# Kernel tuning notes

Hardware: AMD Instinct MI355X
Metric: run time of the kernel (lower is better)

## Reference

```python
import jax, jax.numpy as jnp
import numpy as np

EMBED_DIM = 1024
HEADS = 16
D_HEAD = EMBED_DIM // HEADS
B, S = 4, 2048


def setup_inputs() -> dict:
    key = jax.random.key(0)
    ks = jax.random.split(key, 7)
    scale = 1.0 / np.sqrt(EMBED_DIM)
    inp = {
        "key": jax.random.normal(ks[0], (B, S, EMBED_DIM), jnp.float32),
        "query": jax.random.normal(ks[1], (B, S, EMBED_DIM), jnp.float32),
        "value": jax.random.normal(ks[2], (B, S, EMBED_DIM), jnp.float32),
        # causal boolean mask, broadcastable to [B, H, S, S]
        "mask": jnp.tril(jnp.ones((S, S), dtype=bool))[None, None, :, :] * jnp.ones((B, 1, 1, 1), dtype=bool),
        # nn.Linear weights, stored torch-style as [out_features, in_features]
        "Wq": jax.random.normal(ks[3], (EMBED_DIM, EMBED_DIM), jnp.float32) * scale,
        "Wk": jax.random.normal(ks[4], (EMBED_DIM, EMBED_DIM), jnp.float32) * scale,
        "Wv": jax.random.normal(ks[5], (EMBED_DIM, EMBED_DIM), jnp.float32) * scale,
        "Wo": jax.random.normal(ks[6], (EMBED_DIM, EMBED_DIM), jnp.float32) * scale,
    }
    return inp


def reference(key, query, value, mask, Wq, Wk, Wv, Wo):
    # projections (nn.Linear, bias=False): x @ W.T
    q = query @ Wq.T                                    # [B,S,E]
    k = key @ Wk.T
    v = value @ Wv.T
    # split heads -> [B,H,S,d]
    def split(x):
        return x.reshape(B, S, HEADS, D_HEAD).transpose(0, 2, 1, 3)
    q, k, v = split(q), split(k), split(v)
    # scaled dot-product scores [B,H,S,S]
    scores = jnp.einsum("bhqd,bhkd->bhqk", q, k) / np.sqrt(D_HEAD).astype(np.float32)
    scores = jnp.where(mask, scores, jnp.float32(-1e9))
    attn = jax.nn.softmax(scores, axis=-1)
    # attention output, merge heads
    out = jnp.einsum("bhqk,bhkd->bhqd", attn, v)        # [B,H,S,d]
    out = out.transpose(0, 2, 1, 3).reshape(B, S, EMBED_DIM)
    return out @ Wo.T
```

## Files before the change

kernel.cpp:

```cpp
#include <hip/hip_runtime.h>

#define SEQ 2048
#define EMBED 1024
#define DHEAD 64

typedef _Float16 h8 __attribute__((ext_vector_type(8)));
typedef _Float16 h4 __attribute__((ext_vector_type(4)));
typedef float f4 __attribute__((ext_vector_type(4)));
typedef unsigned int u32;

__device__ __forceinline__ void gload_lds16(const void* g, void* l) {
    __builtin_amdgcn_global_load_lds(
        (const __attribute__((address_space(1))) u32*)g,
        (__attribute__((address_space(3))) u32*)l, 16, 0, 0);
}

__global__ __launch_bounds__(256) void cvt_f16(
    const float* __restrict__ q, const float* __restrict__ k, const float* __restrict__ v,
    const float* __restrict__ wq, const float* __restrict__ wk, const float* __restrict__ wv,
    const float* __restrict__ wo,
    _Float16* __restrict__ q16, _Float16* __restrict__ k16, _Float16* __restrict__ v16,
    _Float16* __restrict__ wq16, _Float16* __restrict__ wk16, _Float16* __restrict__ wv16,
    _Float16* __restrict__ wo16)
{
    int bid = blockIdx.x;
    const float* src;
    _Float16* dst;
    float scale = 1.0f;
    size_t base;
    if (bid < 24576) {
        int seg = bid >> 13;
        base = (size_t)(bid & 8191) * 1024 + threadIdx.x * 4;
        src = seg == 0 ? q : seg == 1 ? k : v;
        dst = seg == 0 ? q16 : seg == 1 ? k16 : v16;
    } else {
        int wb = bid - 24576;
        int seg = wb >> 10;
        base = (size_t)(wb & 1023) * 1024 + threadIdx.x * 4;
        src = seg == 0 ? wq : seg == 1 ? wk : seg == 2 ? wv : wo;
        dst = seg == 0 ? wq16 : seg == 1 ? wk16 : seg == 2 ? wv16 : wo16;
        if (seg == 0) scale = 0.18033688011112042f;
    }
    float4 x = *(const float4*)(src + base);
    h4 y = { (_Float16)(x.x * scale), (_Float16)(x.y * scale),
             (_Float16)(x.z * scale), (_Float16)(x.w * scale) };
    *(h4*)(dst + base) = y;
}

__device__ __forceinline__ void gemm_core(const _Float16* __restrict__ A, const _Float16* __restrict__ W,
                                          int m0, int n0, int tid,
                                          _Float16* As, _Float16* Bs, f4 acc[4][4])
{
    const int lane = tid & 63, wave = tid >> 6;
    const int t16 = lane & 15, quad = lane >> 4;
    const int wm = (wave >> 1) * 64, wn = (wave & 1) * 64;
    const int wb = wave * 64;
    const int u0 = tid, u1 = tid + 256;
    const int r0 = u0 >> 2, c0 = u0 & 3;
    const int r1 = u1 >> 2, c1 = u1 & 3;
    const _Float16* ga0 = A + (size_t)(m0 + r0) * 1024 + c0 * 8;
    const _Float16* ga1 = A + (size_t)(m0 + r1) * 1024 + c1 * 8;
    const _Float16* gb0 = W + (size_t)(n0 + r0) * 1024 + c0 * 8;
    const _Float16* gb1 = W + (size_t)(n0 + r1) * 1024 + c1 * 8;
    _Float16* la0 = As + wb * 8;
    _Float16* la1 = As + (256 + wb) * 8;
    _Float16* lb0 = Bs + wb * 8;
    _Float16* lb1 = Bs + (256 + wb) * 8;

    for (int k0 = 0; k0 < 1024; k0 += 32) {
        __syncthreads();
        gload_lds16(ga0 + k0, la0);
        gload_lds16(ga1 + k0, la1);
        gload_lds16(gb0 + k0, lb0);
        gload_lds16(gb1 + k0, lb1);
        __syncthreads();
        h8 af[4], bf[4];
#pragma unroll
        for (int i = 0; i < 4; ++i)
            af[i] = *(const h8*)(As + (wm + i * 16 + t16) * 32 + quad * 8);
#pragma unroll
        for (int j = 0; j < 4; ++j)
            bf[j] = *(const h8*)(Bs + (wn + j * 16 + t16) * 32 + quad * 8);
#pragma unroll
        for (int i = 0; i < 4; ++i)
#pragma unroll
            for (int j = 0; j < 4; ++j)
                acc[i][j] = __builtin_amdgcn_mfma_f32_16x16x32_f16(af[i], bf[j], acc[i][j], 0, 0, 0);
    }
}

__global__ __launch_bounds__(256) void proj_qkv(
    const _Float16* __restrict__ q16, const _Float16* __restrict__ k16, const _Float16* __restrict__ v16,
    const _Float16* __restrict__ Wq, const _Float16* __restrict__ Wk, const _Float16* __restrict__ Wv,
    _Float16* __restrict__ Qh, _Float16* __restrict__ Kh, _Float16* __restrict__ Vt)
{
    __shared__ _Float16 As[4096], Bs[4096];
    const int tid = threadIdx.x;
    const int z = blockIdx.z;
    const _Float16 *A, *W;
    int m0, n0;
    if (z == 2) { A = Wv; W = v16; m0 = blockIdx.y * 128; n0 = blockIdx.x * 128; }
    else if (z == 0) { A = q16; W = Wq; m0 = blockIdx.x * 128; n0 = blockIdx.y * 128; }
    else { A = k16; W = Wk; m0 = blockIdx.x * 128; n0 = blockIdx.y * 128; }

    f4 acc[4][4];
    const f4 z4 = {0.f, 0.f, 0.f, 0.f};
#pragma unroll
    for (int i = 0; i < 4; ++i)
#pragma unroll
        for (int j = 0; j < 4; ++j) acc[i][j] = z4;

    gemm_core(A, W, m0, n0, tid, As, Bs, acc);

    const int lane = tid & 63, wave = tid >> 6;
    const int t16 = lane & 15, quad = lane >> 4;
    const int wm = (wave >> 1) * 64, wn = (wave & 1) * 64;
#pragma unroll
    for (int i = 0; i < 4; ++i)
#pragma unroll
        for (int j = 0; j < 4; ++j)
#pragma unroll
            for (int reg = 0; reg < 4; ++reg) {
                int gm = m0 + wm + i * 16 + quad * 4 + reg;
                int gn = n0 + wn + j * 16 + t16;
                float vv = acc[i][j][reg];
                if (z < 2) {
                    int b = gm >> 11, s = gm & 2047, h = gn >> 6, dd = gn & 63;
                    _Float16* dst = (z == 0) ? Qh : Kh;
                    dst[(((size_t)(b * 16 + h) * SEQ) + s) * DHEAD + dd] = (_Float16)vv;
                } else {
                    int h = gm >> 6, dd = gm & 63, b = gn >> 11, s = gn & 2047;
                    Vt[(((size_t)(b * 16 + h) * DHEAD) + dd) * SEQ + s] = (_Float16)vv;
                }
            }
}

__global__ __launch_bounds__(256) void attn3(
    const _Float16* __restrict__ Qh, const _Float16* __restrict__ Kh,
    const _Float16* __restrict__ Vt, _Float16* __restrict__ Ob)
{
    __shared__ _Float16 Kbuf[2][8][512];
    __shared__ _Float16 Vbuf[2][8][512];
    __shared__ _Float16 Pex[4][2][512];

    const int tid = threadIdx.x;
    const int lane = tid & 63, wave = tid >> 6;
    const int t16 = lane & 15, quad = lane >> 4;
    const int bh = blockIdx.x;
    const int b = bh >> 4, h = bh & 15;
    const int qb = (gridDim.y - 1) - blockIdx.y;
    const int q0 = qb * 128;
    const int nqt = qb * 2 + 2;

    const _Float16* Qp = Qh + (size_t)bh * SEQ * DHEAD;
    const _Float16* Kp = Kh + (size_t)bh * SEQ * DHEAD;
    const _Float16* Vp = Vt + (size_t)bh * DHEAD * SEQ;

    const int qlo[2] = { q0 + wave * 32, q0 + wave * 32 + 16 };
    const int last0 = (qlo[0] + 15) >> 6;

    h8 qf[2][2];
#pragma unroll
    for (int qb2 = 0; qb2 < 2; ++qb2)
#pragma unroll
        for (int kc = 0; kc < 2; ++kc)
            qf[qb2][kc] = *(const h8*)(Qp + (size_t)(qlo[qb2] + t16) * 64 + kc * 32 + quad * 8);

    const _Float16* Kl = Kp + t16 * 64 + quad * 8;
    const _Float16* Vl = Vp + t16 * 2048 + quad * 8;

#define STAGE(jt_, bufi)                                                                  \
    do {                                                                                  \
        if (wave < 2) {                                                                   \
            _Pragma("unroll")                                                             \
            for (int i_ = 0; i_ < 4; ++i_) {                                              \
                int g_ = wave * 4 + i_;                                                   \
                gload_lds16(Kl + (jt_) * 4096 + (g_ >> 1) * 1024 + (g_ & 1) * 32,         \
                            &Kbuf[bufi][g_][0]);                                          \
            }                                                                             \
        } else {                                                                          \
            _Pragma("unroll")                                                             \
            for (int i_ = 0; i_ < 4; ++i_) {                                              \
                int g_ = (wave - 2) * 4 + i_;                                             \
                gload_lds16(Vl + (g_ >> 1) * 32768 + (jt_) * 64 + (g_ & 1) * 32,          \
                            &Vbuf[bufi][g_][0]);                                          \
            }                                                                             \
        }                                                                                 \
    } while (0)

    STAGE(0, 0);
    __syncthreads();

    float mv[2] = {-1e30f, -1e30f};
    float lv[2] = {0.f, 0.f};
    f4 o_acc[2][4];
    const f4 z4 = {0.f, 0.f, 0.f, 0.f};
#pragma unroll
    for (int qb2 = 0; qb2 < 2; ++qb2)
#pragma unroll
        for (int dt = 0; dt < 4; ++dt) o_acc[qb2][dt] = z4;

    for (int jt = 0; jt < nqt; ++jt) {
        const int buf = jt & 1;
        if (jt + 1 < nqt) STAGE(jt + 1, buf ^ 1);

        if (jt <= last0) {
            f4 s0[4], s1[4];
#pragma unroll
            for (int j4 = 0; j4 < 4; ++j4) {
                h8 kfa = *(const h8*)(&Kbuf[buf][j4 * 2 + 0][lane * 8]);
                h8 kfb = *(const h8*)(&Kbuf[buf][j4 * 2 + 1][lane * 8]);
                s1[j4] = __builtin_amdgcn_mfma_f32_16x16x32_f16(kfa, qf[1][0], z4, 0, 0, 0);
                s1[j4] = __builtin_amdgcn_mfma_f32_16x16x32_f16(kfb, qf[1][1], s1[j4], 0, 0, 0);
                s0[j4] = __builtin_amdgcn_mfma_f32_16x16x32_f16(kfa, qf[0][0], z4, 0, 0, 0);
                s0[j4] = __builtin_amdgcn_mfma_f32_16x16x32_f16(kfb, qf[0][1], s0[j4], 0, 0, 0);
            }

            auto softmax_store = [&](f4* s, int qb2) {
                const int myq = qlo[qb2] + t16;
                if ((jt << 6) + 63 > qlo[qb2]) {
#pragma unroll
                    for (int j4 = 0; j4 < 4; ++j4)
#pragma unroll
                        for (int reg = 0; reg < 4; ++reg) {
                            int kk = (jt << 6) + j4 * 16 + quad * 4 + reg;
                            if (kk > myq) s[j4][reg] = -1e30f;
                        }
                }
                float mr = s[0][0];
#pragma unroll
                for (int j4 = 0; j4 < 4; ++j4)
#pragma unroll
                    for (int reg = 0; reg < 4; ++reg) mr = fmaxf(mr, s[j4][reg]);
                mr = fmaxf(mr, __shfl_xor(mr, 16, 64));
                mr = fmaxf(mr, __shfl_xor(mr, 32, 64));
                float mn = mv[qb2];
                if (__any(mr > mn + 8.0f)) {
                    mn = fmaxf(mn, mr);
                    float al = __builtin_amdgcn_exp2f(mv[qb2] - mn);
                    mv[qb2] = mn;
                    lv[qb2] *= al;
#pragma unroll
                    for (int dt = 0; dt < 4; ++dt)
#pragma unroll
                        for (int reg = 0; reg < 4; ++reg) o_acc[qb2][dt][reg] *= al;
                }
                float rs = 0.f;
#pragma unroll
                for (int j4 = 0; j4 < 4; ++j4) {
#pragma unroll
                    for (int reg = 0; reg < 4; ++reg) {
                        float p = __builtin_amdgcn_exp2f(s[j4][reg] - mn);
                        s[j4][reg] = p;
                        rs += p;
                    }
                    int Lt = (((j4 & 1) * 2 + (quad >> 1)) << 4) + t16;
                    h4 ph = { (_Float16)s[j4][0], (_Float16)s[j4][1],
                              (_Float16)s[j4][2], (_Float16)s[j4][3] };
                    *(h4*)(&Pex[wave][j4 >> 1][Lt * 8 + (quad & 1) * 4]) = ph;
                }
                rs += __shfl_xor(rs, 16, 64);
                rs += __shfl_xor(rs, 32, 64);
                lv[qb2] += rs;
            };

            softmax_store(s0, 0);
            {
                h8 pa = *(const h8*)(&Pex[wave][0][lane * 8]);
                h8 pb = *(const h8*)(&Pex[wave][1][lane * 8]);
#pragma unroll
                for (int dt = 0; dt < 4; ++dt) {
                    h8 ava = *(const h8*)(&Vbuf[buf][dt * 2 + 0][lane * 8]);
                    h8 avb = *(const h8*)(&Vbuf[buf][dt * 2 + 1][lane * 8]);
                    o_acc[0][dt] = __builtin_amdgcn_mfma_f32_16x16x32_f16(ava, pa, o_acc[0][dt], 0, 0, 0);
                    o_acc[0][dt] = __builtin_amdgcn_mfma_f32_16x16x32_f16(avb, pb, o_acc[0][dt], 0, 0, 0);
                }
            }
            softmax_store(s1, 1);
            {
                h8 pa = *(const h8*)(&Pex[wave][0][lane * 8]);
                h8 pb = *(const h8*)(&Pex[wave][1][lane * 8]);
#pragma unroll
                for (int dt = 0; dt < 4; ++dt) {
                    h8 ava = *(const h8*)(&Vbuf[buf][dt * 2 + 0][lane * 8]);
                    h8 avb = *(const h8*)(&Vbuf[buf][dt * 2 + 1][lane * 8]);
                    o_acc[1][dt] = __builtin_amdgcn_mfma_f32_16x16x32_f16(ava, pa, o_acc[1][dt], 0, 0, 0);
                    o_acc[1][dt] = __builtin_amdgcn_mfma_f32_16x16x32_f16(avb, pb, o_acc[1][dt], 0, 0, 0);
                }
            }
        }
        __syncthreads();
    }

#pragma unroll
    for (int qb2 = 0; qb2 < 2; ++qb2) {
        float inv = __builtin_amdgcn_rcpf(lv[qb2]);
        _Float16* ep = &Pex[wave][0][0];
#pragma unroll
        for (int dt = 0; dt < 4; ++dt) {
            h4 ov = { (_Float16)(o_acc[qb2][dt][0] * inv), (_Float16)(o_acc[qb2][dt][1] * inv),
                      (_Float16)(o_acc[qb2][dt][2] * inv), (_Float16)(o_acc[qb2][dt][3] * inv) };
            *(h4*)(ep + t16 * 64 + dt * 16 + quad * 4) = ov;
        }
        h8 r0 = *(const h8*)(ep + t16 * 64 + quad * 8);
        h8 r1 = *(const h8*)(ep + t16 * 64 + 32 + quad * 8);
        int s = qlo[qb2] + t16;
        _Float16* og = Ob + ((size_t)(b * SEQ + s)) * EMBED + h * DHEAD;
        *(h8*)(og + quad * 8) = r0;
        *(h8*)(og + 32 + quad * 8) = r1;
    }
#undef STAGE
}

__global__ __launch_bounds__(256) void proj_out(
    const _Float16* __restrict__ A, const _Float16* __restrict__ Wo, float* __restrict__ out)
{
    __shared__ _Float16 As[4096], Bs[4096];
    const int tid = threadIdx.x;
    const int m0 = blockIdx.x * 128, n0 = blockIdx.y * 128;
    f4 acc[4][4];
    const f4 z4 = {0.f, 0.f, 0.f, 0.f};
#pragma unroll
    for (int i = 0; i < 4; ++i)
#pragma unroll
        for (int j = 0; j < 4; ++j) acc[i][j] = z4;

    gemm_core(A, Wo, m0, n0, tid, As, Bs, acc);

    const int lane = tid & 63, wave = tid >> 6;
    const int t16 = lane & 15, quad = lane >> 4;
    const int wm = (wave >> 1) * 64, wn = (wave & 1) * 64;
#pragma unroll
    for (int i = 0; i < 4; ++i)
#pragma unroll
        for (int j = 0; j < 4; ++j)
#pragma unroll
            for (int reg = 0; reg < 4; ++reg) {
                int gm = m0 + wm + i * 16 + quad * 4 + reg;
                int gn = n0 + wn + j * 16 + t16;
                out[(size_t)gm * EMBED + gn] = acc[i][j][reg];
            }
}

extern "C" void kernel_launch(void* const* d_in, const int* in_sizes, int n_in,
                              void* d_out, int out_size, void* d_ws, size_t ws_size,
                              hipStream_t stream) {
    const float* key   = (const float*)d_in[0];
    const float* query = (const float*)d_in[1];
    const float* value = (const float*)d_in[2];
    const float* Wq = (const float*)d_in[4];
    const float* Wk = (const float*)d_in[5];
    const float* Wv = (const float*)d_in[6];
    const float* Wo = (const float*)d_in[7];

    char* ws = (char*)d_ws;
    _Float16* v16  = (_Float16*)(ws);
    _Float16* Wq16 = (_Float16*)(ws + (16u << 20));
    _Float16* Wk16 = (_Float16*)(ws + (18u << 20));
    _Float16* Wv16 = (_Float16*)(ws + (20u << 20));
    _Float16* Wo16 = (_Float16*)(ws + (22u << 20));
    _Float16* Qh   = (_Float16*)(ws + (24u << 20));
    _Float16* Kh   = (_Float16*)(ws + (40u << 20));
    _Float16* Vt   = (_Float16*)(ws + (56u << 20));
    _Float16* Ob   = v16;
    _Float16* q16 = (_Float16*)d_out;
    _Float16* k16 = (_Float16*)d_out + 8388608;

    dim3 blk(256);
    cvt_f16<<<dim3(28672), blk, 0, stream>>>(query, key, value, Wq, Wk, Wv, Wo,
                                             q16, k16, v16, Wq16, Wk16, Wv16, Wo16);
    proj_qkv<<<dim3(64, 8, 3), blk, 0, stream>>>(q16, k16, v16, Wq16, Wk16, Wv16, Qh, Kh, Vt);
    attn3<<<dim3(64, 16), blk, 0, stream>>>(Qh, Kh, Vt, Ob);
    proj_out<<<dim3(64, 8), blk, 0, stream>>>(Ob, Wo16, (float*)d_out);
}
```

Before: 353.0 us.

## Keep softmax P in registers via 16x16x16 MFMA with pre-swizzled V layout

The V projection epilogue now writes V in a fragment-ordered layout that matches the register layout of the P accumulator. This lets the attention kernel feed the exponentiated scores directly as h4 operands to 16x16x16 MFMAs instead of round-tripping P through the Pex LDS buffer. The epilogue reuses Kbuf as scratch with an XOR swizzle to reduce bank conflicts. The cost is twice as many (smaller) MFMA instructions for PV and a scattered write pattern for V in the projection kernel.

```diff
diff --git a/kernel.cpp b/kernel.cpp
--- a/kernel.cpp
+++ b/kernel.cpp
@@ -130,7 +130,13 @@
                     dst[(((size_t)(b * 16 + h) * SEQ) + s) * DHEAD + dd] = (_Float16)vv;
                 } else {
                     int h = gm >> 6, dd = gm & 63, b = gn >> 11, s = gn & 2047;
-                    Vt[(((size_t)(b * 16 + h) * DHEAD) + dd) * SEQ + s] = (_Float16)vv;
+                    int jt = s >> 6, ks = s & 63;
+                    int j4 = ks >> 4, quadv = (ks >> 2) & 3, regv = ks & 3;
+                    int dt = dd >> 4, t16v = dd & 15;
+                    size_t off = (size_t)(b * 16 + h) * (SEQ * DHEAD)
+                               + (size_t)(jt * 8 + dt * 2 + (j4 >> 1)) * 512
+                               + (quadv * 16 + t16v) * 8 + (j4 & 1) * 4 + regv;
+                    Vt[off] = (_Float16)vv;
                 }
             }
 }
@@ -141,7 +147,6 @@
 {
     __shared__ _Float16 Kbuf[2][8][512];
     __shared__ _Float16 Vbuf[2][8][512];
-    __shared__ _Float16 Pex[4][2][512];
 
     const int tid = threadIdx.x;
     const int lane = tid & 63, wave = tid >> 6;
@@ -154,7 +159,7 @@
 
     const _Float16* Qp = Qh + (size_t)bh * SEQ * DHEAD;
     const _Float16* Kp = Kh + (size_t)bh * SEQ * DHEAD;
-    const _Float16* Vp = Vt + (size_t)bh * DHEAD * SEQ;
+    const _Float16* Vp = Vt + (size_t)bh * SEQ * DHEAD;
 
     const int qlo[2] = { q0 + wave * 32, q0 + wave * 32 + 16 };
     const int last0 = (qlo[0] + 15) >> 6;
@@ -167,7 +172,7 @@
             qf[qb2][kc] = *(const h8*)(Qp + (size_t)(qlo[qb2] + t16) * 64 + kc * 32 + quad * 8);
 
     const _Float16* Kl = Kp + t16 * 64 + quad * 8;
-    const _Float16* Vl = Vp + t16 * 2048 + quad * 8;
+    const _Float16* Vl = Vp + lane * 8;
 
 #define STAGE(jt_, bufi)                                                                  \
     do {                                                                                  \
@@ -182,8 +187,7 @@
             _Pragma("unroll")                                                             \
             for (int i_ = 0; i_ < 4; ++i_) {                                              \
                 int g_ = (wave - 2) * 4 + i_;                                             \
-                gload_lds16(Vl + (g_ >> 1) * 32768 + (jt_) * 64 + (g_ & 1) * 32,          \
-                            &Vbuf[bufi][g_][0]);                                          \
+                gload_lds16(Vl + ((jt_) * 8 + g_) * 512, &Vbuf[bufi][g_][0]);             \
             }                                                                             \
         }                                                                                 \
     } while (0)
@@ -216,7 +220,8 @@
                 s0[j4] = __builtin_amdgcn_mfma_f32_16x16x32_f16(kfb, qf[0][1], s0[j4], 0, 0, 0);
             }
 
-            auto softmax_store = [&](f4* s, int qb2) {
+            h4 pf0[4], pf1[4];
+            auto softmax_frag = [&](f4* s, int qb2, h4* pf) {
                 const int myq = qlo[qb2] + t16;
                 if ((jt << 6) + 63 > qlo[qb2]) {
 #pragma unroll
@@ -254,56 +259,46 @@
                         s[j4][reg] = p;
                         rs += p;
                     }
-                    int Lt = (((j4 & 1) * 2 + (quad >> 1)) << 4) + t16;
-                    h4 ph = { (_Float16)s[j4][0], (_Float16)s[j4][1],
-                              (_Float16)s[j4][2], (_Float16)s[j4][3] };
-                    *(h4*)(&Pex[wave][j4 >> 1][Lt * 8 + (quad & 1) * 4]) = ph;
+                    pf[j4] = (h4){ (_Float16)s[j4][0], (_Float16)s[j4][1],
+                                   (_Float16)s[j4][2], (_Float16)s[j4][3] };
                 }
                 rs += __shfl_xor(rs, 16, 64);
                 rs += __shfl_xor(rs, 32, 64);
                 lv[qb2] += rs;
             };
-
-            softmax_store(s0, 0);
-            {
-                h8 pa = *(const h8*)(&Pex[wave][0][lane * 8]);
-                h8 pb = *(const h8*)(&Pex[wave][1][lane * 8]);
-#pragma unroll
-                for (int dt = 0; dt < 4; ++dt) {
-                    h8 ava = *(const h8*)(&Vbuf[buf][dt * 2 + 0][lane * 8]);
-                    h8 avb = *(const h8*)(&Vbuf[buf][dt * 2 + 1][lane * 8]);
-                    o_acc[0][dt] = __builtin_amdgcn_mfma_f32_16x16x32_f16(ava, pa, o_acc[0][dt], 0, 0, 0);
-                    o_acc[0][dt] = __builtin_amdgcn_mfma_f32_16x16x32_f16(avb, pb, o_acc[0][dt], 0, 0, 0);
-                }
-            }
-            softmax_store(s1, 1);
-            {
-                h8 pa = *(const h8*)(&Pex[wave][0][lane * 8]);
-                h8 pb = *(const h8*)(&Pex[wave][1][lane * 8]);
-#pragma unroll
-                for (int dt = 0; dt < 4; ++dt) {
-                    h8 ava = *(const h8*)(&Vbuf[buf][dt * 2 + 0][lane * 8]);
-                    h8 avb = *(const h8*)(&Vbuf[buf][dt * 2 + 1][lane * 8]);
-                    o_acc[1][dt] = __builtin_amdgcn_mfma_f32_16x16x32_f16(ava, pa, o_acc[1][dt], 0, 0, 0);
-                    o_acc[1][dt] = __builtin_amdgcn_mfma_f32_16x16x32_f16(avb, pb, o_acc[1][dt], 0, 0, 0);
+            softmax_frag(s0, 0, pf0);
+            softmax_frag(s1, 1, pf1);
+
+#pragma unroll
+            for (int dt = 0; dt < 4; ++dt) {
+#pragma unroll
+                for (int j4p = 0; j4p < 2; ++j4p) {
+                    h8 v2 = *(const h8*)(&Vbuf[buf][dt * 2 + j4p][lane * 8]);
+                    h4 vlo = __builtin_shufflevector(v2, v2, 0, 1, 2, 3);
+                    h4 vhi = __builtin_shufflevector(v2, v2, 4, 5, 6, 7);
+                    o_acc[0][dt] = __builtin_amdgcn_mfma_f32_16x16x16f16(vlo, pf0[j4p * 2 + 0], o_acc[0][dt], 0, 0, 0);
+                    o_acc[0][dt] = __builtin_amdgcn_mfma_f32_16x16x16f16(vhi, pf0[j4p * 2 + 1], o_acc[0][dt], 0, 0, 0);
+                    o_acc[1][dt] = __builtin_amdgcn_mfma_f32_16x16x16f16(vlo, pf1[j4p * 2 + 0], o_acc[1][dt], 0, 0, 0);
+                    o_acc[1][dt] = __builtin_amdgcn_mfma_f32_16x16x16f16(vhi, pf1[j4p * 2 + 1], o_acc[1][dt], 0, 0, 0);
                 }
             }
         }
         __syncthreads();
     }
 
+    _Float16* ep = ((_Float16*)Kbuf) + wave * 1024;
+    const int swz = (t16 & 7) << 3;
 #pragma unroll
     for (int qb2 = 0; qb2 < 2; ++qb2) {
         float inv = __builtin_amdgcn_rcpf(lv[qb2]);
-        _Float16* ep = &Pex[wave][0][0];
 #pragma unroll
         for (int dt = 0; dt < 4; ++dt) {
             h4 ov = { (_Float16)(o_acc[qb2][dt][0] * inv), (_Float16)(o_acc[qb2][dt][1] * inv),
                       (_Float16)(o_acc[qb2][dt][2] * inv), (_Float16)(o_acc[qb2][dt][3] * inv) };
-            *(h4*)(ep + t16 * 64 + dt * 16 + quad * 4) = ov;
+            *(h4*)(ep + t16 * 64 + ((dt * 16 + quad * 4) ^ swz)) = ov;
         }
-        h8 r0 = *(const h8*)(ep + t16 * 64 + quad * 8);
-        h8 r1 = *(const h8*)(ep + t16 * 64 + 32 + quad * 8);
+        h8 r0 = *(const h8*)(ep + t16 * 64 + ((quad * 8) ^ swz));
+        h8 r1 = *(const h8*)(ep + t16 * 64 + ((32 + quad * 8) ^ swz));
         int s = qlo[qb2] + t16;
         _Float16* og = Ob + ((size_t)(b * SEQ + s)) * EMBED + h * DHEAD;
         *(h8*)(og + quad * 8) = r0;
```

Measured after the change: 347.4 us. About the same (-1.6%).
